# Optimization experiments

Measured on AMD Instinct MI355X. Metric: run time of the kernel, lower is better.

Reference implementation:

```python
import jax, jax.numpy as jnp
import numpy as np

D_MODEL = 1024
D_STATE = 64
N_HEADS = 16
CHUNK = 64


def segsum(x):
    # x: (..., T) -> (..., T, T) with [i, j] = sum_{j<k<=i} x[k], -inf above diagonal
    T = x.shape[-1]
    xx = jnp.broadcast_to(x[..., None], x.shape + (T,))  # [i, j] = x[i]
    lower = jnp.tril(jnp.ones((T, T), dtype=bool), -1)
    xs = jnp.cumsum(jnp.where(lower, xx, 0.0), axis=-2)
    keep = jnp.tril(jnp.ones((T, T), dtype=bool), 0)
    return jnp.where(keep, xs, -jnp.inf)


def ssd_minimal(X, A, B, C, block_len):
    b, L, h, p = X.shape
    n = B.shape[-1]
    c = L // block_len
    l = block_len
    X = X.reshape(b, c, l, h, p)
    A = A.reshape(b, c, l, h).transpose(0, 3, 1, 2)  # b h c l
    B = B.reshape(b, c, l, h, n)
    C = C.reshape(b, c, l, h, n)
    A_cumsum = jnp.cumsum(A, axis=-1)  # b h c l
    Lmat = jnp.exp(segsum(A))  # b h c l l
    Y_diag = jnp.einsum('bclhn,bcshn,bhcls,bcshp->bclhp', C, B, Lmat, X)
    decay_states = jnp.exp(A_cumsum[:, :, :, -1:] - A_cumsum)  # b h c l
    states = jnp.einsum('bclhn,bhcl,bclhp->bchpn', B, decay_states, X)
    init = jnp.zeros_like(states[:, :1])
    states = jnp.concatenate([init, states], axis=1)  # b (c+1) h p n
    A_last = A_cumsum[:, :, :, -1]  # b h c
    decay_chunk = jnp.exp(segsum(jnp.pad(A_last, ((0, 0), (0, 0), (1, 0)))))  # b h (c+1) (c+1)
    new_states = jnp.einsum('bhzc,bchpn->bzhpn', decay_chunk, states)
    states, final_state = new_states[:, :-1], new_states[:, -1]
    state_decay_out = jnp.exp(A_cumsum)  # b h c l
    Y_off = jnp.einsum('bclhn,bchpn,bhcl->bclhp', C, states, state_decay_out)
    Y = (Y_diag + Y_off).reshape(b, L, h, p)
    return Y, final_state


def mamba2_forward(x, W_in, W_dt, b_dt, W_B, W_C, W_out, A_log):
    b, L, d = x.shape
    h, n = N_HEADS, D_STATE
    p = d // h
    # seqlen divisible by CHUNK -> no padding needed (pad_len == 0)
    xz = x @ W_in.T  # (b, L, 2d)
    x_in, z = xz[..., :d], xz[..., d:]
    dt = jax.nn.softplus(x @ W_dt.T + b_dt)  # (b, L, h)
    A = -jnp.exp(A_log)[None, None, :] * dt  # (b, L, h)
    B = (x @ W_B.T).reshape(b, L, h, n)
    C = (x @ W_C.T).reshape(b, L, h, n)
    X = x_in.reshape(b, L, h, p) * dt[..., None]
    Y, new_state = ssd_minimal(X, A, B, C, CHUNK)
    y = Y.reshape(b, L, d) * jax.nn.silu(z)
    y = y @ W_out.T
    return y, new_state


def setup_inputs() -> dict:
    key = jax.random.key(0)
    ks = jax.random.split(key, 7)
    d, h, n = D_MODEL, N_HEADS, D_STATE
    x = jax.random.normal(ks[0], (2, 4096, d), dtype=jnp.float32)
    # xavier_uniform with gain 0.5 for in/out proj
    lim_in = 0.5 * np.sqrt(6.0 / (d + 2 * d))
    W_in = jax.random.uniform(ks[1], (2 * d, d), minval=-lim_in, maxval=lim_in, dtype=jnp.float32)
    lim_out = 0.5 * np.sqrt(6.0 / (d + d))
    W_out = jax.random.uniform(ks[2], (d, d), minval=-lim_out, maxval=lim_out, dtype=jnp.float32)
    # default torch Linear init (kaiming-uniform-ish): U(-1/sqrt(fan_in), 1/sqrt(fan_in))
    lim = 1.0 / np.sqrt(d)
    W_dt = jax.random.uniform(ks[3], (h, d), minval=-lim, maxval=lim, dtype=jnp.float32)
    b_dt = jnp.zeros((h,), dtype=jnp.float32)
    W_B = jax.random.uniform(ks[4], (h * n, d), minval=-lim, maxval=lim, dtype=jnp.float32)
    W_C = jax.random.uniform(ks[5], (h * n, d), minval=-lim, maxval=lim, dtype=jnp.float32)
    A_log = jnp.log(jnp.linspace(1.0, 16.0, h)).astype(jnp.float32)
    return {"x": x, "W_in": W_in, "W_dt": W_dt, "b_dt": b_dt, "W_B": W_B, "W_C": W_C, "W_out": W_out, "A_log": A_log}


def reference(x, W_in, W_dt, b_dt, W_B, W_C, W_out, A_log):
    return mamba2_forward(x, W_in, W_dt, b_dt, W_B, W_C, W_out, A_log)
```

## Files before the change

kernel.cpp:

```cpp
#include <hip/hip_runtime.h>
#include <cstdint>
#include <cstddef>

#define NTOK 8192

typedef __bf16 bf16x8 __attribute__((ext_vector_type(8)));
typedef float f32x4 __attribute__((ext_vector_type(4)));
typedef float f32x4v __attribute__((ext_vector_type(4)));
typedef unsigned short u16x8 __attribute__((ext_vector_type(8)));

__device__ __forceinline__ float b2f(unsigned short u) {
    return __uint_as_float(((unsigned int)u) << 16);
}
__device__ __forceinline__ unsigned short f2b(float f) {
    unsigned int u = __float_as_uint(f);
    u += 0x7FFFu + ((u >> 16) & 1u);
    return (unsigned short)(u >> 16);
}

__device__ __forceinline__ void async_lds16(unsigned short* lds, const unsigned short* g) {
    __builtin_amdgcn_global_load_lds(
        (const __attribute__((address_space(1))) unsigned int*)g,
        (__attribute__((address_space(3))) unsigned int*)lds,
        16, 0, 0);
}

__global__ __launch_bounds__(256) void f32_to_bf16(
    const float* __restrict__ in, unsigned short* __restrict__ out, int n8)
{
    const int i = blockIdx.x * 256 + threadIdx.x;
    if (i >= n8) return;
    const f32x4v* p = (const f32x4v*)(in + (long)i * 8);
    f32x4v a = p[0], b = p[1];
    u16x8 v;
#pragma unroll
    for (int t = 0; t < 4; t++) { v[t] = f2b(a[t]); v[t + 4] = f2b(b[t]); }
    *(u16x8*)(out + (long)i * 8) = v;
}

__global__ void scalars16(const float* __restrict__ a, const float* __restrict__ b,
                          float* __restrict__ alogf, float* __restrict__ bdtf) {
    if (threadIdx.x == 0) {
        float ma = 0.f, mb = 0.f;
        for (int i = 0; i < 16; i++) { ma = fmaxf(ma, fabsf(a[i])); mb = fmaxf(mb, fabsf(b[i])); }
        const float* alog = (ma >= mb) ? a : b;
        const float* bdt  = (ma >= mb) ? b : a;
        for (int i = 0; i < 16; i++) { alogf[i] = alog[i]; bdtf[i] = bdt[i]; }
    }
}

__global__ __launch_bounds__(256) void dt_kernel(
    const float* __restrict__ x, const float* __restrict__ Wdt,
    const float* __restrict__ bdt, const float* __restrict__ Alog,
    float* __restrict__ dtp, float* __restrict__ Ap)
{
    const int token = blockIdx.x * 16 + (threadIdx.x >> 4);
    const int h = threadIdx.x & 15;
    const f32x4v* xr = (const f32x4v*)(x + (long)token * 1024);
    const f32x4v* wr = (const f32x4v*)(Wdt + h * 1024);
    float s0 = bdt[h], s1 = 0.f;
#pragma unroll 8
    for (int k = 0; k < 256; k += 2) {
        f32x4v a0 = xr[k], w0 = wr[k];
        f32x4v a1 = xr[k + 1], w1 = wr[k + 1];
        s0 += a0[0] * w0[0] + a0[1] * w0[1] + a0[2] * w0[2] + a0[3] * w0[3];
        s1 += a1[0] * w1[0] + a1[1] * w1[1] + a1[2] * w1[2] + a1[3] * w1[3];
    }
    const float s = s0 + s1;
    const float dtv = (s > 15.f) ? s : log1pf(expf(s));
    dtp[token * 16 + h] = dtv;
    Ap[token * 16 + h] = -expf(Alog[h]) * dtv;
}

template <int MODE, int OUT32>
__global__ __launch_bounds__(256) void gemm_bf16(
    const unsigned short* __restrict__ A, const unsigned short* __restrict__ W,
    int N, int K,
    void* __restrict__ out0, unsigned short* __restrict__ out1,
    const float* __restrict__ dtp)
{
    __shared__ unsigned short As[128 * 64];
    __shared__ unsigned short Ws[128 * 64];

    const int tid = threadIdx.x;
    const int lane = tid & 63;
    const int warp = tid >> 6;
    const long arow0 = (long)blockIdx.y * 128;
    const long wrow0 = (long)blockIdx.x * 128;

    const int mw = (warp >> 1) * 64;
    const int nw = (warp & 1) * 64;
    const int qm = lane & 15;
    const int quad = lane >> 4;

    f32x4 acc[4][4];
    const f32x4 zero = {0.f, 0.f, 0.f, 0.f};
#pragma unroll
    for (int i = 0; i < 4; i++)
#pragma unroll
        for (int j = 0; j < 4; j++) acc[i][j] = zero;

    const int e0 = tid * 8;
    const int srow = e0 >> 6, scol = e0 & 63;

    for (int k0 = 0; k0 < K; k0 += 64) {
        __syncthreads();
#pragma unroll
        for (int r = 0; r < 4; r++) {
            const int e = r * 2048 + e0;
            const int row = r * 32 + srow;
            async_lds16(As + e, A + (arow0 + row) * (long)K + k0 + scol);
            async_lds16(Ws + e, W + (wrow0 + row) * (long)K + k0 + scol);
        }
        __syncthreads();
#pragma unroll
        for (int kk = 0; kk < 64; kk += 32) {
            bf16x8 fa[4], fb[4];
#pragma unroll
            for (int mi = 0; mi < 4; mi++)
                fa[mi] = *(const bf16x8*)(As + (mw + mi * 16 + qm) * 64 + kk + quad * 8);
#pragma unroll
            for (int ni = 0; ni < 4; ni++)
                fb[ni] = *(const bf16x8*)(Ws + (nw + ni * 16 + qm) * 64 + kk + quad * 8);
#pragma unroll
            for (int mi = 0; mi < 4; mi++)
#pragma unroll
                for (int ni = 0; ni < 4; ni++)
                    acc[mi][ni] = __builtin_amdgcn_mfma_f32_16x16x32_bf16(
                        fa[mi], fb[ni], acc[mi][ni], 0, 0, 0);
        }
    }
#pragma unroll
    for (int mi = 0; mi < 4; mi++)
#pragma unroll
        for (int ni = 0; ni < 4; ni++)
#pragma unroll
            for (int r = 0; r < 4; r++) {
                const long row = arow0 + mw + mi * 16 + quad * 4 + r;
                const long col = wrow0 + nw + ni * 16 + qm;
                const float v = acc[mi][ni][r];
                if (MODE == 0) {
                    if (OUT32) ((float*)out0)[row * N + col] = v;
                    else ((unsigned short*)out0)[row * N + col] = f2b(v);
                } else if (MODE == 1) {
                    if (col < 1024) {
                        ((unsigned short*)out0)[row * 1024 + col] = f2b(v * dtp[row * 16 + (int)(col >> 6)]);
                    } else {
                        out1[row * 1024 + (col - 1024)] = f2b(v / (1.f + expf(-v)));
                    }
                } else {
                    if (col < 1024) ((unsigned short*)out0)[row * 1024 + col] = f2b(v);
                    else out1[row * 1024 + (col - 1024)] = f2b(v);
                }
            }
}

__global__ __launch_bounds__(256) void ssd_states(
    const unsigned short* __restrict__ Xb, const unsigned short* __restrict__ Bb,
    const float* __restrict__ Ap, float* __restrict__ st_out,
    float* __restrict__ Alast)
{
    __shared__ __align__(16) unsigned short Xh[64 * 64];
    __shared__ __align__(16) unsigned short Xl[64 * 64];
    __shared__ __align__(16) unsigned short Bt[64 * 64];
    __shared__ float Acum[64];
    __shared__ float dec[64];

    const int blk = blockIdx.x;
    const int h = blk & 15;
    const int c = (blk >> 4) & 63;
    const int b = blk >> 10;
    const long tokenbase = (long)b * 4096 + (long)c * 64;
    const int tid = threadIdx.x;
    const int lane = tid & 63;
    const int w = tid >> 6;
    const int qm = lane & 15;
    const int quad = lane >> 4;

    if (tid < 64) Acum[tid] = Ap[(tokenbase + tid) * 16 + h];

    const int row = tid & 63;
    u16x8 rx[2], rb[2];
#pragma unroll
    for (int i = 0; i < 2; i++) {
        const int ch = (tid >> 6) + 4 * i;
        const long g = (tokenbase + row) * 1024 + h * 64 + ch * 8;
        rx[i] = *(const u16x8*)(Xb + g);
        rb[i] = *(const u16x8*)(Bb + g);
    }
    __syncthreads();
    if (tid == 0) {
        float s = 0.f;
        for (int l = 0; l < 64; l++) { s += Acum[l]; Acum[l] = s; }
        Alast[(b * 16 + h) * 64 + c] = s;
    }
    __syncthreads();
    if (tid < 64) dec[tid] = expf(Acum[63] - Acum[tid]);
    __syncthreads();

    const float dv = dec[row];
#pragma unroll
    for (int i = 0; i < 2; i++) {
        const int ch = (tid >> 6) + 4 * i;
#pragma unroll
        for (int t = 0; t < 8; t++) {
            const int pn = ch * 8 + t;
            const int d = (pn * 64 + row) ^ (t << 3);
            const float xd = b2f(rx[i][t]) * dv;
            const unsigned short hi = f2b(xd);
            Xh[d] = hi;
            Xl[d] = f2b(xd - b2f(hi));
            Bt[d] = rb[i][t];
        }
    }
    __syncthreads();

    f32x4 acc[4];
    const f32x4 zero = {0.f, 0.f, 0.f, 0.f};
#pragma unroll
    for (int ni = 0; ni < 4; ni++) acc[ni] = zero;
#pragma unroll
    for (int kk2 = 0; kk2 < 2; kk2++) {
        const int ko = kk2 * 32 + quad * 8;
        const int ra = 16 * w + qm;
        const int da = (ra * 64 + ko) ^ ((ra & 7) << 3);
        bf16x8 fxh = *(const bf16x8*)(Xh + da);
        bf16x8 fxl = *(const bf16x8*)(Xl + da);
#pragma unroll
        for (int ni = 0; ni < 4; ni++) {
            const int rn = ni * 16 + qm;
            bf16x8 fb = *(const bf16x8*)(Bt + ((rn * 64 + ko) ^ ((rn & 7) << 3)));
            acc[ni] = __builtin_amdgcn_mfma_f32_16x16x32_bf16(fxh, fb, acc[ni], 0, 0, 0);
            acc[ni] = __builtin_amdgcn_mfma_f32_16x16x32_bf16(fxl, fb, acc[ni], 0, 0, 0);
        }
    }
    const long sbase = (long)blk * 4096;
    const int p0 = 16 * w + quad * 4;
#pragma unroll
    for (int ni = 0; ni < 4; ni++)
#pragma unroll
        for (int r = 0; r < 4; r++)
            st_out[sbase + (p0 + r) * 64 + ni * 16 + qm] = acc[ni][r];
}

__global__ __launch_bounds__(256) void scan_kernel(
    float* __restrict__ st, const float* __restrict__ Alast)
{
    const int blk = blockIdx.x;
    const int grp = blk & 15;
    const int h = (blk >> 4) & 15;
    const int b = blk >> 8;
    const int e = grp * 256 + threadIdx.x;
    const float* al = Alast + (b * 16 + h) * 64;
    float M = 0.f;
    for (int c = 0; c < 64; c++) {
        const long idx = ((long)((b * 64 + c) * 16 + h)) * 4096 + e;
        const float s = st[idx];
        st[idx] = M;
        M = expf(al[c]) * M + s;
    }
    st[(long)8388608 + (long)(b * 16 + h) * 4096 + e] = M;
}

__global__ __launch_bounds__(256) void ssd_yoff(
    const unsigned short* __restrict__ Xb, const unsigned short* __restrict__ Bb,
    const unsigned short* __restrict__ Cb, const float* __restrict__ Ap,
    const float* __restrict__ st, unsigned short* __restrict__ SZb)
{
    __shared__ __align__(16) unsigned short Bs[64 * 64];
    __shared__ __align__(16) unsigned short Ss[64 * 64];
    __shared__ __align__(16) unsigned short Xt[64 * 64];
    __shared__ __align__(16) unsigned short Gs[64 * 64];
    __shared__ float Acum[64];

    const int blk = blockIdx.x;
    const int h = blk & 15;
    const int c = (blk >> 4) & 63;
    const int b = blk >> 10;
    const long tokenbase = (long)b * 4096 + (long)c * 64;
    const int tid = threadIdx.x;
    const int lane = tid & 63;
    const int w = tid >> 6;
    const int qm = lane & 15;
    const int quad = lane >> 4;
    const long sbase = (long)blk * 4096;

    if (tid < 64) Acum[tid] = Ap[(tokenbase + tid) * 16 + h];

#pragma unroll
    for (int i = 0; i < 2; i++) {
        const int idx = tid + i * 256;
        const int r8 = idx >> 3, c8 = (idx & 7) * 8;
        const long g = (tokenbase + r8) * 1024 + h * 64 + c8;
        const int d = (r8 * 64 + c8) ^ ((r8 & 7) << 3);
        *(u16x8*)(Bs + d) = *(const u16x8*)(Bb + g);
        const float* sp = st + sbase + r8 * 64 + c8;
        f32x4v s0 = *(const f32x4v*)sp, s1 = *(const f32x4v*)(sp + 4);
        u16x8 sv;
#pragma unroll
        for (int t = 0; t < 4; t++) { sv[t] = f2b(s0[t]); sv[t + 4] = f2b(s1[t]); }
        *(u16x8*)(Ss + d) = sv;
    }
    const int xrow = tid & 63;
#pragma unroll
    for (int i = 0; i < 2; i++) {
        const int ch = (tid >> 6) + 4 * i;
        const long g = (tokenbase + xrow) * 1024 + h * 64 + ch * 8;
        u16x8 xv = *(const u16x8*)(Xb + g);
#pragma unroll
        for (int t = 0; t < 8; t++) {
            const int p = ch * 8 + t;
            Xt[(p * 64 + xrow) ^ (t << 3)] = xv[t];
        }
    }
    u16x8 fc[2];
#pragma unroll
    for (int kk2 = 0; kk2 < 2; kk2++)
        fc[kk2] = *(const u16x8*)(Cb + (tokenbase + 16 * w + qm) * 1024 + h * 64 + kk2 * 32 + quad * 8);

    __syncthreads();
    if (tid == 0) {
        float s = 0.f;
        for (int l = 0; l < 64; l++) { s += Acum[l]; Acum[l] = s; }
    }

    f32x4 acc1[4], acc2[4];
    const f32x4 zero = {0.f, 0.f, 0.f, 0.f};
#pragma unroll
    for (int ni = 0; ni < 4; ni++) { acc1[ni] = zero; acc2[ni] = zero; }
#pragma unroll
    for (int kk2 = 0; kk2 < 2; kk2++) {
        const int ko = kk2 * 32 + quad * 8;
        bf16x8 fa = *(const bf16x8*)&fc[kk2];
#pragma unroll
        for (int ni = 0; ni < 4; ni++) {
            const int rn = ni * 16 + qm;
            const int d = (rn * 64 + ko) ^ ((rn & 7) << 3);
            bf16x8 fbb = *(const bf16x8*)(Bs + d);
            acc1[ni] = __builtin_amdgcn_mfma_f32_16x16x32_bf16(fa, fbb, acc1[ni], 0, 0, 0);
            bf16x8 fbs = *(const bf16x8*)(Ss + d);
            acc2[ni] = __builtin_amdgcn_mfma_f32_16x16x32_bf16(fa, fbs, acc2[ni], 0, 0, 0);
        }
    }
    __syncthreads();

    const int l0 = 16 * w + quad * 4;
    float al[4];
#pragma unroll
    for (int r = 0; r < 4; r++) al[r] = Acum[l0 + r];
#pragma unroll
    for (int ni = 0; ni < 4; ni++) {
        const int s = ni * 16 + qm;
        const float as = Acum[s];
#pragma unroll
        for (int r = 0; r < 4; r++) {
            const int l = l0 + r;
            const float gv = (s <= l) ? acc1[ni][r] * expf(al[r] - as) : 0.f;
            Gs[(l * 64 + s) ^ ((l & 7) << 3)] = f2b(gv);
        }
    }
    __syncthreads();

    f32x4 acc3[4];
#pragma unroll
    for (int ni = 0; ni < 4; ni++) acc3[ni] = zero;
#pragma unroll
    for (int kk2 = 0; kk2 < 2; kk2++) {
        const int ko = kk2 * 32 + quad * 8;
        const int ra = 16 * w + qm;
        bf16x8 fg = *(const bf16x8*)(Gs + ((ra * 64 + ko) ^ ((ra & 7) << 3)));
#pragma unroll
        for (int ni = 0; ni < 4; ni++) {
            const int rp = ni * 16 + qm;
            bf16x8 fx = *(const bf16x8*)(Xt + ((rp * 64 + ko) ^ ((rp & 7) << 3)));
            acc3[ni] = __builtin_amdgcn_mfma_f32_16x16x32_bf16(fg, fx, acc3[ni], 0, 0, 0);
        }
    }
    float eds[4];
#pragma unroll
    for (int r = 0; r < 4; r++) eds[r] = expf(al[r]);
#pragma unroll
    for (int ni = 0; ni < 4; ni++) {
#pragma unroll
        for (int r = 0; r < 4; r++) {
            const int l = l0 + r;
            const int p = ni * 16 + qm;
            const float Y = acc3[ni][r] + eds[r] * acc2[ni][r];
            const long o = (tokenbase + l) * 1024 + h * 64 + p;
            SZb[o] = f2b(Y * b2f(SZb[o]));
        }
    }
}

extern "C" void kernel_launch(void* const* d_in, const int* in_sizes, int n_in,
                              void* d_out, int out_size, void* d_ws, size_t ws_size,
                              hipStream_t stream)
{
    int ix = 0, iwin = 1, iwdt = 2, i1m[3] = {4, 5, 6}, n1m = 0, i16[2] = {3, 7}, n16 = 0;
    for (int i = 0; i < n_in; i++) {
        switch (in_sizes[i]) {
            case 8388608: ix = i; break;
            case 2097152: iwin = i; break;
            case 16384:   iwdt = i; break;
            case 1048576: if (n1m < 3) i1m[n1m++] = i; break;
            case 16:      if (n16 < 2) i16[n16++] = i; break;
            default: break;
        }
    }
    if (n1m < 3) { i1m[0] = 4; i1m[1] = 5; i1m[2] = 6; }
    if (n16 < 2) { i16[0] = 3; i16[1] = 7; }
    const float* x     = (const float*)d_in[ix];
    const float* W_in  = (const float*)d_in[iwin];
    const float* W_dt  = (const float*)d_in[iwdt];
    const float* W_B   = (const float*)d_in[i1m[0]];
    const float* W_C   = (const float*)d_in[i1m[1]];
    const float* W_out = (const float*)d_in[i1m[2]];
    const float* s16a  = (const float*)d_in[i16[0]];
    const float* s16b  = (const float*)d_in[i16[1]];
    float* out = (float*)d_out;

    char* ws = (char*)d_ws;
    float* dtp   = (float*)(ws);
    float* Ap    = (float*)(ws + 524288);
    float* Alast = (float*)(ws + 1048576);
    float* Alogf = (float*)(ws + 1056768);
    float* bdtf  = (float*)(ws + 1056832);
    unsigned short* Xb  = (unsigned short*)(ws + 2097152);
    unsigned short* Bb  = (unsigned short*)(ws + 18874368);
    unsigned short* Cb  = (unsigned short*)(ws + 35651584);
    unsigned short* SZb = (unsigned short*)(ws + 52428800);

    unsigned short* xb  = (unsigned short*)d_out;
    unsigned short* Wib = (unsigned short*)((char*)d_out + 16777216);
    unsigned short* Wbc = (unsigned short*)((char*)d_out + 20971520);
    unsigned short* Wob = Xb;

    float* states = out;

    scalars16<<<1, 64, 0, stream>>>(s16a, s16b, Alogf, bdtf);
    f32_to_bf16<<<4096, 256, 0, stream>>>(x, xb, 1048576);
    f32_to_bf16<<<1024, 256, 0, stream>>>(W_in, Wib, 262144);
    f32_to_bf16<<<512, 256, 0, stream>>>(W_B, Wbc, 131072);
    f32_to_bf16<<<512, 256, 0, stream>>>(W_C, Wbc + 1048576, 131072);
    dt_kernel<<<NTOK / 16, 256, 0, stream>>>(x, W_dt, bdtf, Alogf, dtp, Ap);
    gemm_bf16<1, 0><<<dim3(16, 64), 256, 0, stream>>>(xb, Wib, 2048, 1024, Xb, SZb, dtp);
    gemm_bf16<2, 0><<<dim3(16, 64), 256, 0, stream>>>(xb, Wbc, 2048, 1024, Bb, Cb, nullptr);
    ssd_states<<<2048, 256, 0, stream>>>(Xb, Bb, Ap, states, Alast);
    scan_kernel<<<512, 256, 0, stream>>>(states, Alast);
    ssd_yoff<<<2048, 256, 0, stream>>>(Xb, Bb, Cb, Ap, states, SZb);
    f32_to_bf16<<<512, 256, 0, stream>>>(W_out, Wob, 131072);
    gemm_bf16<0, 1><<<dim3(8, 64), 256, 0, stream>>>(SZb, Wob, 1024, 1024, out, nullptr, nullptr);
}
```

Baseline: 393.5 us.

## Merge input projections into one 256x256-tile double-buffered GEMM with block swizzle

Replaces the 128x128 single-buffered bf16 GEMM with a 256x256 tile, 512-thread kernel that double-buffers LDS loads so global-to-LDS copies overlap MFMA work. It also fuses the W_in and W_B/W_C projections into a single GEMM over a stacked 4096-row weight, and remaps block IDs with an XCD-aware swizzle. The aim is more operand reuse per tile, fewer launches, and latency hiding. In exchange it uses 128KB of LDS per block, which limits occupancy, and the output projection now runs on only 128 blocks.

```diff
diff --git a/kernel.cpp b/kernel.cpp
--- a/kernel.cpp
+++ b/kernel.cpp
@@ -72,85 +72,106 @@
     Ap[token * 16 + h] = -expf(Alog[h]) * dtv;
 }
 
-template <int MODE, int OUT32>
-__global__ __launch_bounds__(256) void gemm_bf16(
+template <int MODE>
+__global__ __launch_bounds__(512, 2) void gemm256(
     const unsigned short* __restrict__ A, const unsigned short* __restrict__ W,
-    int N, int K,
+    const int NT_N, const int N, const int K,
     void* __restrict__ out0, unsigned short* __restrict__ out1,
+    unsigned short* __restrict__ out2, unsigned short* __restrict__ out3,
     const float* __restrict__ dtp)
 {
-    __shared__ unsigned short As[128 * 64];
-    __shared__ unsigned short Ws[128 * 64];
+    __shared__ unsigned short As[2][256 * 64];
+    __shared__ unsigned short Ws[2][256 * 64];
 
     const int tid = threadIdx.x;
     const int lane = tid & 63;
     const int warp = tid >> 6;
-    const long arow0 = (long)blockIdx.y * 128;
-    const long wrow0 = (long)blockIdx.x * 128;
-
-    const int mw = (warp >> 1) * 64;
-    const int nw = (warp & 1) * 64;
+    const int wm = warp >> 2;
+    const int wn = warp & 3;
     const int qm = lane & 15;
     const int quad = lane >> 4;
 
-    f32x4 acc[4][4];
+    const int nwg = gridDim.x;
+    const int cpx = nwg >> 3;
+    const int bid = blockIdx.x;
+    const int swz = (bid & 7) * cpx + (bid >> 3);
+    const int bx = swz % NT_N;
+    const int by = swz / NT_N;
+    const long arow0 = (long)by * 256;
+    const long wrow0 = (long)bx * 256;
+
+    const int srow = tid >> 3;
+    const int scol = (tid & 7) * 8;
+
+    f32x4 acc[8][4];
     const f32x4 zero = {0.f, 0.f, 0.f, 0.f};
 #pragma unroll
-    for (int i = 0; i < 4; i++)
+    for (int i = 0; i < 8; i++)
 #pragma unroll
         for (int j = 0; j < 4; j++) acc[i][j] = zero;
 
-    const int e0 = tid * 8;
-    const int srow = e0 >> 6, scol = e0 & 63;
-
-    for (int k0 = 0; k0 < K; k0 += 64) {
-        __syncthreads();
+    auto stage = [&](int buf, int k0) {
 #pragma unroll
         for (int r = 0; r < 4; r++) {
-            const int e = r * 2048 + e0;
-            const int row = r * 32 + srow;
-            async_lds16(As + e, A + (arow0 + row) * (long)K + k0 + scol);
-            async_lds16(Ws + e, W + (wrow0 + row) * (long)K + k0 + scol);
-        }
-        __syncthreads();
+            const int e = r * 4096 + tid * 8;
+            const int row = r * 64 + srow;
+            async_lds16(As[buf] + e, A + (arow0 + row) * (long)K + k0 + scol);
+            async_lds16(Ws[buf] + e, W + (wrow0 + row) * (long)K + k0 + scol);
+        }
+    };
+    auto compute = [&](const unsigned short* Ab, const unsigned short* Wb) {
 #pragma unroll
         for (int kk = 0; kk < 64; kk += 32) {
-            bf16x8 fa[4], fb[4];
-#pragma unroll
-            for (int mi = 0; mi < 4; mi++)
-                fa[mi] = *(const bf16x8*)(As + (mw + mi * 16 + qm) * 64 + kk + quad * 8);
+            bf16x8 fa[8], fb[4];
+#pragma unroll
+            for (int mi = 0; mi < 8; mi++)
+                fa[mi] = *(const bf16x8*)(Ab + (wm * 128 + mi * 16 + qm) * 64 + kk + quad * 8);
 #pragma unroll
             for (int ni = 0; ni < 4; ni++)
-                fb[ni] = *(const bf16x8*)(Ws + (nw + ni * 16 + qm) * 64 + kk + quad * 8);
-#pragma unroll
-            for (int mi = 0; mi < 4; mi++)
+                fb[ni] = *(const bf16x8*)(Wb + (wn * 64 + ni * 16 + qm) * 64 + kk + quad * 8);
+#pragma unroll
+            for (int mi = 0; mi < 8; mi++)
 #pragma unroll
                 for (int ni = 0; ni < 4; ni++)
                     acc[mi][ni] = __builtin_amdgcn_mfma_f32_16x16x32_bf16(
                         fa[mi], fb[ni], acc[mi][ni], 0, 0, 0);
         }
-    }
-#pragma unroll
-    for (int mi = 0; mi < 4; mi++)
+    };
+
+    const int nk = K >> 6;
+    int cur = 0;
+    stage(0, 0);
+    __syncthreads();
+    for (int t = 1; t < nk; t++) {
+        stage(cur ^ 1, t << 6);
+        compute(As[cur], Ws[cur]);
+        __syncthreads();
+        cur ^= 1;
+    }
+    compute(As[cur], Ws[cur]);
+
+#pragma unroll
+    for (int mi = 0; mi < 8; mi++)
 #pragma unroll
         for (int ni = 0; ni < 4; ni++)
 #pragma unroll
             for (int r = 0; r < 4; r++) {
-                const long row = arow0 + mw + mi * 16 + quad * 4 + r;
-                const long col = wrow0 + nw + ni * 16 + qm;
+                const long row = arow0 + wm * 128 + mi * 16 + quad * 4 + r;
+                const int col = (int)wrow0 + wn * 64 + ni * 16 + qm;
                 const float v = acc[mi][ni][r];
                 if (MODE == 0) {
-                    if (OUT32) ((float*)out0)[row * N + col] = v;
-                    else ((unsigned short*)out0)[row * N + col] = f2b(v);
-                } else if (MODE == 1) {
-                    if (col < 1024) {
-                        ((unsigned short*)out0)[row * 1024 + col] = f2b(v * dtp[row * 16 + (int)(col >> 6)]);
+                    ((float*)out0)[row * N + col] = v;
+                } else {
+                    const int seg = col >> 10, cc = col & 1023;
+                    if (seg == 0) {
+                        ((unsigned short*)out0)[row * 1024 + cc] = f2b(v * dtp[row * 16 + (cc >> 6)]);
+                    } else if (seg == 1) {
+                        out1[row * 1024 + cc] = f2b(v / (1.f + expf(-v)));
+                    } else if (seg == 2) {
+                        out2[row * 1024 + cc] = f2b(v);
                     } else {
-                        out1[row * 1024 + (col - 1024)] = f2b(v / (1.f + expf(-v)));
+                        out3[row * 1024 + cc] = f2b(v);
                     }
-                } else {
-                    if (col < 1024) ((unsigned short*)out0)[row * 1024 + col] = f2b(v);
-                    else out1[row * 1024 + (col - 1024)] = f2b(v);
                 }
             }
 }
@@ -431,23 +452,21 @@
     unsigned short* SZb = (unsigned short*)(ws + 52428800);
 
     unsigned short* xb  = (unsigned short*)d_out;
-    unsigned short* Wib = (unsigned short*)((char*)d_out + 16777216);
-    unsigned short* Wbc = (unsigned short*)((char*)d_out + 20971520);
+    unsigned short* Wst = (unsigned short*)((char*)d_out + 16777216);
     unsigned short* Wob = Xb;
 
     float* states = out;
 
     scalars16<<<1, 64, 0, stream>>>(s16a, s16b, Alogf, bdtf);
     f32_to_bf16<<<4096, 256, 0, stream>>>(x, xb, 1048576);
-    f32_to_bf16<<<1024, 256, 0, stream>>>(W_in, Wib, 262144);
-    f32_to_bf16<<<512, 256, 0, stream>>>(W_B, Wbc, 131072);
-    f32_to_bf16<<<512, 256, 0, stream>>>(W_C, Wbc + 1048576, 131072);
+    f32_to_bf16<<<1024, 256, 0, stream>>>(W_in, Wst, 262144);
+    f32_to_bf16<<<512, 256, 0, stream>>>(W_B, Wst + 2097152, 131072);
+    f32_to_bf16<<<512, 256, 0, stream>>>(W_C, Wst + 3145728, 131072);
     dt_kernel<<<NTOK / 16, 256, 0, stream>>>(x, W_dt, bdtf, Alogf, dtp, Ap);
-    gemm_bf16<1, 0><<<dim3(16, 64), 256, 0, stream>>>(xb, Wib, 2048, 1024, Xb, SZb, dtp);
-    gemm_bf16<2, 0><<<dim3(16, 64), 256, 0, stream>>>(xb, Wbc, 2048, 1024, Bb, Cb, nullptr);
+    gemm256<1><<<512, 512, 0, stream>>>(xb, Wst, 16, 4096, 1024, Xb, SZb, Bb, Cb, dtp);
     ssd_states<<<2048, 256, 0, stream>>>(Xb, Bb, Ap, states, Alast);
     scan_kernel<<<512, 256, 0, stream>>>(states, Alast);
     ssd_yoff<<<2048, 256, 0, stream>>>(Xb, Bb, Cb, Ap, states, SZb);
     f32_to_bf16<<<512, 256, 0, stream>>>(W_out, Wob, 131072);
-    gemm_bf16<0, 1><<<dim3(8, 64), 256, 0, stream>>>(SZb, Wob, 1024, 1024, out, nullptr, nullptr);
-}
+    gemm256<0><<<128, 512, 0, stream>>>(SZb, Wob, 4, 1024, 1024, out, nullptr, nullptr, nullptr, nullptr);
+}
```

Measured after the change: 427.8 us. 1.09x slower.
